# Optimization experiments

Measured on AMD Instinct MI355X. Metric: run time of the kernel, lower is better.

The kernel has to match this reference:

```python
import jax, jax.numpy as jnp
import numpy as np

BN_EPS = 1e-5


def conv1x1(x, W, b):
    # x: [B, Cin, N], W: [Cout, Cin], b: [Cout]
    return jnp.einsum('oc,bcn->bon', W, x) + b[None, :, None]


def bn(x, p):
    # p: [4, C] rows = gamma, beta, running_mean, running_var (inference BN)
    g, be, m, v = p[0], p[1], p[2], p[3]
    inv = jax.lax.rsqrt(v + BN_EPS)
    return (x - m[None, :, None]) * (g * inv)[None, :, None] + be[None, :, None]


def conv_bn_relu(x, W, b, p):
    return jax.nn.relu(bn(conv1x1(x, W, b), p))


def _make_params(key, cout, cin):
    k1, k2 = jax.random.split(key)
    W = jax.random.normal(k1, (cout, cin), jnp.float32) * (1.0 / np.sqrt(cin))
    b = jax.random.normal(k2, (cout,), jnp.float32) * 0.01
    p = jnp.stack([jnp.ones(cout), jnp.zeros(cout), jnp.zeros(cout), jnp.ones(cout)]).astype(jnp.float32)
    return W, b, p


def setup_inputs() -> dict:
    key = jax.random.key(0)
    ks = jax.random.split(key, 16)
    B, N, S, D1, D2 = 2, 16384, 4096, 128, 256
    Cin, C, Cm = D1 + D2 + 13, 128, 128  # 397, out_channel, mlp[0]
    inp = {
        'xyz1': jax.random.normal(ks[0], (B, N, 3), jnp.float32),
        'xyz2': jax.random.normal(ks[1], (B, S, 3), jnp.float32),
        'points1': jax.random.normal(ks[2], (B, D1, N), jnp.float32),
        'points2': jax.random.normal(ks[3], (B, D2, S), jnp.float32),
        'last_pred': jax.random.normal(ks[4], (B, S, 13), jnp.float32),
    }
    inp['fuse_W'], inp['fuse_b'], inp['fuse_bn'] = _make_params(ks[5], C, Cin)
    inp['ext1_W'], inp['ext1_b'], inp['ext1_bn'] = _make_params(ks[6], C, C)
    inp['ext2_W'], inp['ext2_b'], inp['ext2_bn'] = _make_params(ks[7], C, C)
    inp['pred1_W'], inp['pred1_b'], inp['pred1_bn'] = _make_params(ks[8], Cm, C)
    inp['pred2_W'], inp['pred2_b'], inp['pred2_bn'] = _make_params(ks[9], 13, Cm)
    return inp


def _forward(xyz1, xyz2, points1, points2, last_pred,
             fuse_W, fuse_b, fuse_bn, ext1_W, ext1_b, ext1_bn,
             ext2_W, ext2_b, ext2_bn, pred1_W, pred1_b, pred1_bn,
             pred2_W, pred2_b, pred2_bn):
    B, N, _ = xyz1.shape
    p1 = jnp.transpose(points1, (0, 2, 1))  # [B, N, D1]
    p2 = jnp.transpose(points2, (0, 2, 1))  # [B, S, D2]
    # squared distances [B, N, S]
    dists = (jnp.sum(xyz1 ** 2, -1)[:, :, None]
             + jnp.sum(xyz2 ** 2, -1)[:, None, :]
             - 2.0 * jnp.einsum('bnc,bsc->bns', xyz1, xyz2))
    # 3 smallest distances (partial top-k instead of full sort; same math)
    neg_d3, idx = jax.lax.top_k(-dists, 3)  # [B, N, 3]
    d3 = -neg_d3
    recip = 1.0 / (d3 + 1e-8)
    weight = recip / jnp.sum(recip, axis=2, keepdims=True)  # [B, N, 3]
    bidx = jnp.arange(B)[:, None, None]
    interp_pts = jnp.sum(p2[bidx, idx] * weight[..., None], axis=2)        # [B, N, D2]
    interp_pred = jnp.sum(last_pred[bidx, idx] * weight[..., None], axis=2)  # [B, N, 13]
    new_points = jnp.transpose(jnp.concatenate([p1, interp_pts, interp_pred], axis=-1), (0, 2, 1))  # [B, Cin, N]
    # fuse
    x = conv_bn_relu(new_points, fuse_W, fuse_b, fuse_bn)
    # extraction: one ConvBNReLURes1D block (groups=1, res_expansion=1)
    h = conv_bn_relu(x, ext1_W, ext1_b, ext1_bn)
    x = jax.nn.relu(bn(conv1x1(h, ext2_W, ext2_b), ext2_bn) + x)  # [B, C, N]
    new_points_out = x
    # prediction head (dropout is identity in eval mode)
    feat = conv_bn_relu(x, pred1_W, pred1_b, pred1_bn)
    pred = conv_bn_relu(feat, pred2_W, pred2_b, pred2_bn)
    return (new_points_out,
            jnp.transpose(feat, (0, 2, 1)),
            jnp.transpose(pred, (0, 2, 1)))


def reference(xyz1, xyz2, points1, points2, last_pred,
              fuse_W, fuse_b, fuse_bn, ext1_W, ext1_b, ext1_bn,
              ext2_W, ext2_b, ext2_bn, pred1_W, pred1_b, pred1_bn,
              pred2_W, pred2_b, pred2_bn):
    return _forward(xyz1, xyz2, points1, points2, last_pred,
                    fuse_W, fuse_b, fuse_bn, ext1_W, ext1_b, ext1_bn,
                    ext2_W, ext2_b, ext2_bn, pred1_W, pred1_b, pred1_bn,
                    pred2_W, pred2_b, pred2_bn)
```

## Files before the change

### kernel.cpp

```cpp
#include <hip/hip_runtime.h>
#include <stdint.h>

#define B_   2
#define N_   16384
#define S_   4096
#define D2_  256
#define CIN_ 397
#define KP_  416
#define C_   128
#define OC_  13
#define NCHUNK_ 16
#define CHS_ (S_ / NCHUNK_)
#define NCAND_ (NCHUNK_ * 3)
#define XBI_P 296

typedef unsigned short u16;
typedef unsigned int u32;
typedef short s16x8 __attribute__((ext_vector_type(8)));
typedef float f32x4 __attribute__((ext_vector_type(4)));

#define MFMA16(a, b, c) __builtin_amdgcn_mfma_f32_16x16x32_bf16((a), (b), (c), 0, 0, 0)

__device__ __forceinline__ float b2f(u16 h) {
  union { unsigned int u; float f; } v; v.u = ((unsigned int)h) << 16; return v.f;
}
__device__ __forceinline__ u16 f2b(float f) {
  union { float f; unsigned int u; } v; v.f = f;
  unsigned int r = v.u + 0x7fffu + ((v.u >> 16) & 1u);
  return (u16)(r >> 16);
}

#define INS3U32(k0, k1, k2, key)            \
  do {                                      \
    u32 _t1 = max(k0, key);                 \
    u32 _t2 = max(k1, key);                 \
    k0 = min(k0, key);                      \
    k1 = min(k1, _t1);                      \
    k2 = min(k2, _t2);                      \
  } while (0)

__device__ __forceinline__ void transpose_body(
    const float* __restrict__ in, u16* __restrict__ out,
    int C, int S, int opitch, int b, int s0, int c0,
    float* __restrict__ tile, int tr, int tc4) {
  const float* ip = in + (size_t)b * C * S;
  u16* op = out + (size_t)b * S * opitch;
#pragma unroll
  for (int r = 0; r < 64; r += 16) {
    float4 v = *(const float4*)(ip + (size_t)(c0 + tr + r) * S + s0 + tc4);
    tile[(tr + r) * 65 + tc4 + 0] = v.x;
    tile[(tr + r) * 65 + tc4 + 1] = v.y;
    tile[(tr + r) * 65 + tc4 + 2] = v.z;
    tile[(tr + r) * 65 + tc4 + 3] = v.w;
  }
  __syncthreads();
#pragma unroll
  for (int r = 0; r < 64; r += 16) {
    ushort4 v;
    v.x = f2b(tile[(tc4 + 0) * 65 + tr + r]);
    v.y = f2b(tile[(tc4 + 1) * 65 + tr + r]);
    v.z = f2b(tile[(tc4 + 2) * 65 + tr + r]);
    v.w = f2b(tile[(tc4 + 3) * 65 + tr + r]);
    *(ushort4*)(op + (size_t)(s0 + tr + r) * opitch + c0 + tc4) = v;
  }
}

__global__ __launch_bounds__(256) void setup_scan_kernel(
    const float* __restrict__ xyz1, const float* __restrict__ xyz2,
    const float* __restrict__ points1, const float* __restrict__ points2,
    const float* __restrict__ fW, const float* __restrict__ fb,
    const float* __restrict__ fbn,
    const float* __restrict__ e1W, const float* __restrict__ e1b,
    const float* __restrict__ e1bn,
    const float* __restrict__ e2W, const float* __restrict__ e2b,
    const float* __restrict__ e2bn,
    const float* __restrict__ p1W, const float* __restrict__ p1b,
    const float* __restrict__ p1bn,
    const float* __restrict__ p2W, const float* __restrict__ p2b,
    const float* __restrict__ p2bn,
    u16* __restrict__ cand, u16* __restrict__ npT, u16* __restrict__ p2t,
    u16* __restrict__ Wf, u16* __restrict__ W1o,
    u16* __restrict__ W2o, u16* __restrict__ W3o,
    u16* __restrict__ Wp2, float* __restrict__ st) {
  __shared__ __align__(16) float smem[64 * 65];
  int id = blockIdx.x;
  int tid = threadIdx.x;

  if (id < 2048) {
    float4* pts = (float4*)smem;
    int chunk = id & 15;
    int ny = (id >> 4) & 63;
    int b = id >> 10;
    int s0 = chunk * CHS_;
    const float* x2 = xyz2 + ((size_t)b * S_ + s0) * 3;
    {
      float xx = x2[tid * 3], yy = x2[tid * 3 + 1], zz = x2[tid * 3 + 2];
      pts[tid] = make_float4(xx, yy, zz, fmaf(xx, xx, fmaf(yy, yy, zz * zz)));
    }
    __syncthreads();
    int n = ny * 256 + tid;
    const float* x1 = xyz1 + ((size_t)b * N_ + n) * 3;
    float ax = x1[0], ay = x1[1], az = x1[2];
    float n1 = fmaf(ax, ax, fmaf(ay, ay, az * az));
    u32 a0k = 0xFFFFFFFFu, a1k = 0xFFFFFFFFu, a2k = 0xFFFFFFFFu;
    u32 b0k = 0xFFFFFFFFu, b1k = 0xFFFFFFFFu, b2k = 0xFFFFFFFFu;
#pragma unroll 4
    for (int s = 0; s < CHS_; s += 2) {
      float4 p = pts[s];
      float4 q = pts[s + 1];
      float dp = fmaf(ax, p.x, fmaf(ay, p.y, az * p.z));
      float dq = fmaf(ax, q.x, fmaf(ay, q.y, az * q.z));
      float da = fmaxf(fmaf(-2.f, dp, n1 + p.w), 0.f);
      float db = fmaxf(fmaf(-2.f, dq, n1 + q.w), 0.f);
      u32 ka = (__float_as_uint(da) & 0xFFFFFF00u) | (u32)s;
      u32 kb = (__float_as_uint(db) & 0xFFFFFF00u) | (u32)(s + 1);
      INS3U32(a0k, a1k, a2k, ka);
      INS3U32(b0k, b1k, b2k, kb);
    }
    INS3U32(a0k, a1k, a2k, b0k);
    INS3U32(a0k, a1k, a2k, b1k);
    INS3U32(a0k, a1k, a2k, b2k);
    u16* co = cand + ((size_t)(b * N_ + n)) * NCAND_ + chunk * 3;
    co[0] = (u16)((a0k & 0xFFu) + s0);
    co[1] = (u16)((a1k & 0xFFu) + s0);
    co[2] = (u16)((a2k & 0xFFu) + s0);
    return;
  }

  int tr = tid >> 4;
  int tc4 = (tid & 15) * 4;
  if (id < 3072) {
    int id2 = id - 2048;
    int sx = id2 & 255, sy = (id2 >> 8) & 1, b = id2 >> 9;
    transpose_body(points1, npT, 128, N_, 128, b, sx * 64, sy * 64, smem, tr, tc4);
    return;
  }
  if (id < 3584) {
    int id2 = id - 3072;
    int sx = id2 & 63, sy = (id2 >> 6) & 3, b = id2 >> 8;
    transpose_body(points2, p2t, 256, S_, 256, b, sx * 64, sy * 64, smem, tr, tc4);
    return;
  }
  int t = (id - 3584) * 256 + tid;
  int stride = 64 * 256;
  for (int i = t; i < 128 * KP_; i += stride) {
    int m = i / KP_, k = i - m * KP_;
    Wf[i] = (k < CIN_) ? f2b(fW[m * CIN_ + k]) : (u16)0;
  }
  for (int i = t; i < 128 * 128; i += stride) {
    W1o[i] = f2b(e1W[i]);
    W2o[i] = f2b(e2W[i]);
    W3o[i] = f2b(p1W[i]);
  }
  for (int i = t; i < 16 * 128; i += stride) {
    int m = i >> 7;
    Wp2[i] = (m < OC_) ? f2b(p2W[i]) : (u16)0;
  }
  for (int i = t; i < 5 * 128; i += stride) {
    int sg = i >> 7, c = i & 127;
    const float* bn; const float* bc; int Cc = 128;
    switch (sg) {
      case 0: bn = fbn;  bc = fb;  break;
      case 1: bn = e1bn; bc = e1b; break;
      case 2: bn = e2bn; bc = e2b; break;
      case 3: bn = p1bn; bc = p1b; break;
      default: bn = p2bn; bc = p2b; Cc = OC_; break;
    }
    float s = 0.f, tt = 0.f;
    if (c < Cc) {
      float g  = bn[0 * Cc + c], be = bn[1 * Cc + c];
      float mu = bn[2 * Cc + c], vv = bn[3 * Cc + c];
      float inv = 1.0f / sqrtf(vv + 1e-5f);
      s = g * inv;
      tt = (bc[c] - mu) * s + be;
    }
    st[sg * 256 + c] = s;
    st[sg * 256 + 128 + c] = tt;
  }
}

__device__ __forceinline__ void ins3(double d, int i,
                                     double& D0, double& D1, double& D2,
                                     int& I0, int& I1, int& I2) {
  if ((d < D2) || (d == D2 && i < I2)) {
    if ((d < D1) || (d == D1 && i < I1)) {
      D2 = D1; I2 = I1;
      if ((d < D0) || (d == D0 && i < I0)) { D1 = D0; I1 = I0; D0 = d; I0 = i; }
      else                                  { D1 = d; I1 = i; }
    } else { D2 = d; I2 = i; }
  }
}

__device__ __forceinline__ void gemm32(const u16* __restrict__ W, const u16* xb,
                                       int l15, int lq, int wv, f32x4 acc[2][2]) {
#pragma unroll
  for (int mtl = 0; mtl < 2; ++mtl) {
    acc[mtl][0] = (f32x4){0.f, 0.f, 0.f, 0.f};
    acc[mtl][1] = (f32x4){0.f, 0.f, 0.f, 0.f};
  }
#pragma unroll
  for (int ks = 0; ks < 4; ++ks) {
    int ko = ks * 32 + lq * 8;
    s16x8 b0 = *(const s16x8*)(xb + l15 * 136 + ko);
    s16x8 b1 = *(const s16x8*)(xb + (16 + l15) * 136 + ko);
#pragma unroll
    for (int mtl = 0; mtl < 2; ++mtl) {
      s16x8 a = *(const s16x8*)(W + (size_t)((wv * 2 + mtl) * 16 + l15) * 128 + ko);
      acc[mtl][0] = MFMA16(a, b0, acc[mtl][0]);
      acc[mtl][1] = MFMA16(a, b1, acc[mtl][1]);
    }
  }
}

__global__ __launch_bounds__(256, 4) void mega_kernel(
    const float* __restrict__ xyz1, const float* __restrict__ xyz2,
    const u16* __restrict__ cand,
    const u16* __restrict__ npT, const u16* __restrict__ p2t,
    const float* __restrict__ last_pred,
    const u16* __restrict__ Wf,
    const u16* __restrict__ W1, const u16* __restrict__ W2,
    const u16* __restrict__ W3, const u16* __restrict__ Wp2,
    const float* __restrict__ st, float* __restrict__ out) {
  __shared__ __align__(16) u16 xb0[32 * 136];
  __shared__ __align__(16) u16 xb1[32 * 136];
  __shared__ u16 xbi[32 * XBI_P];
  __shared__ float wL[32][3];
  __shared__ int   iL[32][3];
  int b = blockIdx.y;
  int n0 = blockIdx.x * 32;
  int tid = threadIdx.x;
  int wv = tid >> 6, lane = tid & 63;
  int l15 = lane & 15, lq = lane >> 4;
  f32x4 acc[2][2];

  {
#pragma clang fp contract(off)
    double* md = (double*)xb0;
    int*    mi = (int*)xb1;
    int qi = tid >> 3, part = tid & 7;
    int qg = b * N_ + n0 + qi;
    const u16* ci = cand + (size_t)qg * NCAND_ + part * 6;
    const float* x2b = xyz2 + (size_t)b * S_ * 3;
    int ii[6];
#pragma unroll
    for (int j = 0; j < 6; ++j) ii[j] = ci[j];
    float pcx[6], pcy[6], pcz[6];
#pragma unroll
    for (int j = 0; j < 6; ++j) {
      const float* p = x2b + (size_t)ii[j] * 3;
      pcx[j] = p[0]; pcy[j] = p[1]; pcz[j] = p[2];
    }
    const float* x1 = xyz1 + (size_t)qg * 3;
    double ax = x1[0], ay = x1[1], az = x1[2];
    double n1 = (ax * ax + ay * ay) + az * az;
    double D0 = 1e300, D1 = 1e300, D2v = 1e300;
    int I0 = 2147483647, I1 = 2147483647, I2 = 2147483647;
#pragma unroll
    for (int j = 0; j < 6; ++j) {
      double px = pcx[j], py = pcy[j], pz = pcz[j];
      double n2 = (px * px + py * py) + pz * pz;
      double dot = (ax * px + ay * py) + az * pz;
      double d = (n1 + n2) - 2.0 * dot;
      ins3(d, ii[j], D0, D1, D2v, I0, I1, I2);
    }
    md[qi * 24 + part * 3 + 0] = D0; mi[qi * 24 + part * 3 + 0] = I0;
    md[qi * 24 + part * 3 + 1] = D1; mi[qi * 24 + part * 3 + 1] = I1;
    md[qi * 24 + part * 3 + 2] = D2v; mi[qi * 24 + part * 3 + 2] = I2;
  }
  __syncthreads();

  if (tid < 32) {
#pragma clang fp contract(off)
    double* md = (double*)xb0;
    int*    mi = (int*)xb1;
    double D0 = 1e300, D1 = 1e300, D2v = 1e300;
    int I0 = 2147483647, I1 = 2147483647, I2 = 2147483647;
    for (int j = 0; j < 24; ++j) {
      ins3(md[tid * 24 + j], mi[tid * 24 + j], D0, D1, D2v, I0, I1, I2);
    }
    double r0 = 1.0 / (D0 + 1e-8);
    double r1 = 1.0 / (D1 + 1e-8);
    double r2 = 1.0 / (D2v + 1e-8);
    double sum = (r0 + r1) + r2;
    wL[tid][0] = (float)(r0 / sum);
    wL[tid][1] = (float)(r1 / sum);
    wL[tid][2] = (float)(r2 / sum);
    iL[tid][0] = I0; iL[tid][1] = I1; iL[tid][2] = I2;
  }
  __syncthreads();

  {
    const float* lpb = last_pred + (size_t)b * S_ * OC_;
    const u16* p2b = p2t + (size_t)b * S_ * D2_;
    ushort4 g0[8], g1[8], g2[8];
#pragma unroll
    for (int i = 0; i < 8; ++i) {
      int p = wv * 8 + i;
      int i0 = iL[p][0], i1 = iL[p][1], i2 = iL[p][2];
      g0[i] = *(const ushort4*)(p2b + (size_t)i0 * D2_ + lane * 4);
      g1[i] = *(const ushort4*)(p2b + (size_t)i1 * D2_ + lane * 4);
      g2[i] = *(const ushort4*)(p2b + (size_t)i2 * D2_ + lane * 4);
    }
#pragma unroll
    for (int i = 0; i < 8; ++i) {
      int p = wv * 8 + i;
      float w0 = wL[p][0], w1 = wL[p][1], w2 = wL[p][2];
      ushort4 v;
      v.x = f2b((w0 * b2f(g0[i].x) + w1 * b2f(g1[i].x)) + w2 * b2f(g2[i].x));
      v.y = f2b((w0 * b2f(g0[i].y) + w1 * b2f(g1[i].y)) + w2 * b2f(g2[i].y));
      v.z = f2b((w0 * b2f(g0[i].z) + w1 * b2f(g1[i].z)) + w2 * b2f(g2[i].z));
      v.w = f2b((w0 * b2f(g0[i].w) + w1 * b2f(g1[i].w)) + w2 * b2f(g2[i].w));
      *(ushort4*)(&xbi[p * XBI_P + lane * 4]) = v;
      if (lane < 32) {
        u16 pv = 0;
        if (lane < OC_) {
          int i0 = iL[p][0], i1 = iL[p][1], i2 = iL[p][2];
          pv = f2b((w0 * lpb[i0 * OC_ + lane] + w1 * lpb[i1 * OC_ + lane])
                   + w2 * lpb[i2 * OC_ + lane]);
        }
        xbi[p * XBI_P + 256 + lane] = pv;
      }
    }
  }
  __syncthreads();

#pragma unroll
  for (int mtl = 0; mtl < 2; ++mtl) {
    acc[mtl][0] = (f32x4){0.f, 0.f, 0.f, 0.f};
    acc[mtl][1] = (f32x4){0.f, 0.f, 0.f, 0.f};
  }
  {
    const u16* brow0 = npT + ((size_t)(b * N_ + n0 + l15)) * 128;
    const u16* brow1 = brow0 + (size_t)16 * 128;
#pragma unroll 1
    for (int ks = 0; ks < 4; ++ks) {
      int ko = ks * 32 + lq * 8;
      s16x8 bf0 = *(const s16x8*)(brow0 + ko);
      s16x8 bf1 = *(const s16x8*)(brow1 + ko);
#pragma unroll
      for (int mtl = 0; mtl < 2; ++mtl) {
        s16x8 a = *(const s16x8*)(Wf + (size_t)((wv * 2 + mtl) * 16 + l15) * KP_ + ko);
        acc[mtl][0] = MFMA16(a, bf0, acc[mtl][0]);
        acc[mtl][1] = MFMA16(a, bf1, acc[mtl][1]);
      }
    }
#pragma unroll 1
    for (int ks = 0; ks < 9; ++ks) {
      int kk = ks * 32 + lq * 8;
      s16x8 bf0 = *(const s16x8*)(&xbi[l15 * XBI_P + kk]);
      s16x8 bf1 = *(const s16x8*)(&xbi[(16 + l15) * XBI_P + kk]);
#pragma unroll
      for (int mtl = 0; mtl < 2; ++mtl) {
        s16x8 a = *(const s16x8*)(Wf + (size_t)((wv * 2 + mtl) * 16 + l15) * KP_ + 128 + kk);
        acc[mtl][0] = MFMA16(a, bf0, acc[mtl][0]);
        acc[mtl][1] = MFMA16(a, bf1, acc[mtl][1]);
      }
    }
  }
#pragma unroll
  for (int mtl = 0; mtl < 2; ++mtl) {
    int m4 = (wv * 2 + mtl) * 16 + lq * 4;
    f32x4 sc = *(const f32x4*)(st + 0 * 256 + m4);
    f32x4 bi = *(const f32x4*)(st + 0 * 256 + 128 + m4);
#pragma unroll
    for (int nt = 0; nt < 2; ++nt) {
      int n_l = nt * 16 + l15;
      ushort4 v;
      v.x = f2b(fmaxf(acc[mtl][nt][0] * sc[0] + bi[0], 0.f));
      v.y = f2b(fmaxf(acc[mtl][nt][1] * sc[1] + bi[1], 0.f));
      v.z = f2b(fmaxf(acc[mtl][nt][2] * sc[2] + bi[2], 0.f));
      v.w = f2b(fmaxf(acc[mtl][nt][3] * sc[3] + bi[3], 0.f));
      *(ushort4*)(&xb0[n_l * 136 + m4]) = v;
    }
  }
  __syncthreads();

  gemm32(W1, xb0, l15, lq, wv, acc);
#pragma unroll
  for (int mtl = 0; mtl < 2; ++mtl) {
    int m4 = (wv * 2 + mtl) * 16 + lq * 4;
    f32x4 sc = *(const f32x4*)(st + 1 * 256 + m4);
    f32x4 bi = *(const f32x4*)(st + 1 * 256 + 128 + m4);
#pragma unroll
    for (int nt = 0; nt < 2; ++nt) {
      int n_l = nt * 16 + l15;
      ushort4 v;
      v.x = f2b(fmaxf(acc[mtl][nt][0] * sc[0] + bi[0], 0.f));
      v.y = f2b(fmaxf(acc[mtl][nt][1] * sc[1] + bi[1], 0.f));
      v.z = f2b(fmaxf(acc[mtl][nt][2] * sc[2] + bi[2], 0.f));
      v.w = f2b(fmaxf(acc[mtl][nt][3] * sc[3] + bi[3], 0.f));
      *(ushort4*)(&xb1[n_l * 136 + m4]) = v;
    }
  }
  __syncthreads();

  gemm32(W2, xb1, l15, lq, wv, acc);
#pragma unroll
  for (int mtl = 0; mtl < 2; ++mtl) {
    int m4 = (wv * 2 + mtl) * 16 + lq * 4;
    f32x4 sc = *(const f32x4*)(st + 2 * 256 + m4);
    f32x4 bi = *(const f32x4*)(st + 2 * 256 + 128 + m4);
#pragma unroll
    for (int nt = 0; nt < 2; ++nt) {
      int n_l = nt * 16 + l15;
      int n_g = n0 + n_l;
      ushort4 xp = *(const ushort4*)(&xb0[n_l * 136 + m4]);
      float v0 = fmaxf(acc[mtl][nt][0] * sc[0] + bi[0] + b2f(xp.x), 0.f);
      float v1 = fmaxf(acc[mtl][nt][1] * sc[1] + bi[1] + b2f(xp.y), 0.f);
      float v2 = fmaxf(acc[mtl][nt][2] * sc[2] + bi[2] + b2f(xp.z), 0.f);
      float v3 = fmaxf(acc[mtl][nt][3] * sc[3] + bi[3] + b2f(xp.w), 0.f);
      ushort4 v;
      v.x = f2b(v0); v.y = f2b(v1); v.z = f2b(v2); v.w = f2b(v3);
      *(ushort4*)(&xb0[n_l * 136 + m4]) = v;
      out[((size_t)(b * C_ + m4 + 0)) * N_ + n_g] = v0;
      out[((size_t)(b * C_ + m4 + 1)) * N_ + n_g] = v1;
      out[((size_t)(b * C_ + m4 + 2)) * N_ + n_g] = v2;
      out[((size_t)(b * C_ + m4 + 3)) * N_ + n_g] = v3;
    }
  }
  __syncthreads();

  gemm32(W3, xb0, l15, lq, wv, acc);
  {
    float* out1 = out + (size_t)B_ * C_ * N_;
#pragma unroll
    for (int mtl = 0; mtl < 2; ++mtl) {
      int m4 = (wv * 2 + mtl) * 16 + lq * 4;
      f32x4 sc = *(const f32x4*)(st + 3 * 256 + m4);
      f32x4 bi = *(const f32x4*)(st + 3 * 256 + 128 + m4);
#pragma unroll
      for (int nt = 0; nt < 2; ++nt) {
        int n_l = nt * 16 + l15;
        int n_g = n0 + n_l;
        float v0 = fmaxf(acc[mtl][nt][0] * sc[0] + bi[0], 0.f);
        float v1 = fmaxf(acc[mtl][nt][1] * sc[1] + bi[1], 0.f);
        float v2 = fmaxf(acc[mtl][nt][2] * sc[2] + bi[2], 0.f);
        float v3 = fmaxf(acc[mtl][nt][3] * sc[3] + bi[3], 0.f);
        ushort4 v;
        v.x = f2b(v0); v.y = f2b(v1); v.z = f2b(v2); v.w = f2b(v3);
        *(ushort4*)(&xb1[n_l * 136 + m4]) = v;
        float4 o4 = make_float4(v0, v1, v2, v3);
        *(float4*)(out1 + ((size_t)(b * N_ + n_g)) * 128 + m4) = o4;
      }
    }
  }
  __syncthreads();

  if (wv < 2) {
    f32x4 a2 = (f32x4){0.f, 0.f, 0.f, 0.f};
#pragma unroll
    for (int ks = 0; ks < 4; ++ks) {
      int ko = ks * 32 + lq * 8;
      s16x8 b0 = *(const s16x8*)(&xb1[(wv * 16 + l15) * 136 + ko]);
      s16x8 a = *(const s16x8*)(Wp2 + (size_t)l15 * 128 + ko);
      a2 = MFMA16(a, b0, a2);
    }
    float* out2 = out + (size_t)B_ * C_ * N_ + (size_t)B_ * N_ * 128;
    f32x4 sc = *(const f32x4*)(st + 4 * 256 + lq * 4);
    f32x4 bi = *(const f32x4*)(st + 4 * 256 + 128 + lq * 4);
    int n_g = n0 + wv * 16 + l15;
#pragma unroll
    for (int r = 0; r < 4; ++r) {
      int m = lq * 4 + r;
      if (m < OC_) {
        out2[((size_t)(b * N_ + n_g)) * OC_ + m] =
            fmaxf(a2[r] * sc[r] + bi[r], 0.f);
      }
    }
  }
}

extern "C" void kernel_launch(void* const* d_in, const int* in_sizes, int n_in,
                              void* d_out, int out_size, void* d_ws, size_t ws_size,
                              hipStream_t stream) {
  const float* xyz1      = (const float*)d_in[0];
  const float* xyz2      = (const float*)d_in[1];
  const float* points1   = (const float*)d_in[2];
  const float* points2   = (const float*)d_in[3];
  const float* last_pred = (const float*)d_in[4];
  const float* fuse_W    = (const float*)d_in[5];
  const float* fuse_b    = (const float*)d_in[6];
  const float* fuse_bn   = (const float*)d_in[7];
  const float* ext1_W    = (const float*)d_in[8];
  const float* ext1_b    = (const float*)d_in[9];
  const float* ext1_bn   = (const float*)d_in[10];
  const float* ext2_W    = (const float*)d_in[11];
  const float* ext2_b    = (const float*)d_in[12];
  const float* ext2_bn   = (const float*)d_in[13];
  const float* pred1_W   = (const float*)d_in[14];
  const float* pred1_b   = (const float*)d_in[15];
  const float* pred1_bn  = (const float*)d_in[16];
  const float* pred2_W   = (const float*)d_in[17];
  const float* pred2_b   = (const float*)d_in[18];
  const float* pred2_bn  = (const float*)d_in[19];

  char* ws = (char*)d_ws;
  u16*   npT  = (u16*)(ws + 0);
  u16*   p2t  = (u16*)(ws + 8388608);
  u16*   cand = (u16*)(ws + 12582912);
  u16*   Wf   = (u16*)(ws + 15728640);
  u16*   W1   = (u16*)(ws + 15835136);
  u16*   W2   = (u16*)(ws + 15867904);
  u16*   W3   = (u16*)(ws + 15900672);
  u16*   Wp2  = (u16*)(ws + 15933440);
  float* st   = (float*)(ws + 15937536);

  setup_scan_kernel<<<dim3(3648), dim3(256), 0, stream>>>(
      xyz1, xyz2, points1, points2,
      fuse_W, fuse_b, fuse_bn, ext1_W, ext1_b, ext1_bn, ext2_W, ext2_b, ext2_bn,
      pred1_W, pred1_b, pred1_bn, pred2_W, pred2_b, pred2_bn,
      cand, npT, p2t, Wf, W1, W2, W3, Wp2, st);

  mega_kernel<<<dim3(N_ / 32, B_), dim3(256), 0, stream>>>(
      xyz1, xyz2, cand, npT, p2t, last_pred,
      Wf, W1, W2, W3, Wp2, st, (float*)d_out);
}
```

Baseline: 204.8 us.

## Double queries per scan thread and replace LDS top-3 merge with shuffles

The scan kernel now handles two query points per thread against each staged xyz2 chunk, halving scan blocks and reusing each LDS point load twice. In the mega kernel, the per-query top-3 merge across 8 threads is done with xor shuffles instead of shared-memory staging plus a single-lane serial merge, which removes two block barriers. Indices and weights are broadcast with readlane. The points1 tile loads are prefetched at kernel start to overlap the gather phase, at the cost of more registers and possibly lower occupancy.

```diff
diff --git a/kernel.cpp b/kernel.cpp
--- a/kernel.cpp
+++ b/kernel.cpp
@@ -86,11 +86,11 @@
   int id = blockIdx.x;
   int tid = threadIdx.x;
 
-  if (id < 2048) {
+  if (id < 1024) {
     float4* pts = (float4*)smem;
     int chunk = id & 15;
-    int ny = (id >> 4) & 63;
-    int b = id >> 10;
+    int ny = (id >> 4) & 31;
+    int b = id >> 9;
     int s0 = chunk * CHS_;
     const float* x2 = xyz2 + ((size_t)b * S_ + s0) * 3;
     {
@@ -98,50 +98,69 @@
       pts[tid] = make_float4(xx, yy, zz, fmaf(xx, xx, fmaf(yy, yy, zz * zz)));
     }
     __syncthreads();
-    int n = ny * 256 + tid;
-    const float* x1 = xyz1 + ((size_t)b * N_ + n) * 3;
-    float ax = x1[0], ay = x1[1], az = x1[2];
-    float n1 = fmaf(ax, ax, fmaf(ay, ay, az * az));
-    u32 a0k = 0xFFFFFFFFu, a1k = 0xFFFFFFFFu, a2k = 0xFFFFFFFFu;
-    u32 b0k = 0xFFFFFFFFu, b1k = 0xFFFFFFFFu, b2k = 0xFFFFFFFFu;
-#pragma unroll 4
+    int nA = ny * 512 + tid;
+    int nB = nA + 256;
+    const float* x1a = xyz1 + ((size_t)b * N_ + nA) * 3;
+    const float* x1b = xyz1 + ((size_t)b * N_ + nB) * 3;
+    float axA = x1a[0], ayA = x1a[1], azA = x1a[2];
+    float axB = x1b[0], ayB = x1b[1], azB = x1b[2];
+    float n1A = fmaf(axA, axA, fmaf(ayA, ayA, azA * azA));
+    float n1B = fmaf(axB, axB, fmaf(ayB, ayB, azB * azB));
+    u32 a0 = ~0u, a1 = ~0u, a2 = ~0u, b0 = ~0u, b1 = ~0u, b2 = ~0u;
+    u32 c0 = ~0u, c1 = ~0u, c2 = ~0u, d0 = ~0u, d1 = ~0u, d2 = ~0u;
+#pragma unroll 2
     for (int s = 0; s < CHS_; s += 2) {
       float4 p = pts[s];
       float4 q = pts[s + 1];
-      float dp = fmaf(ax, p.x, fmaf(ay, p.y, az * p.z));
-      float dq = fmaf(ax, q.x, fmaf(ay, q.y, az * q.z));
-      float da = fmaxf(fmaf(-2.f, dp, n1 + p.w), 0.f);
-      float db = fmaxf(fmaf(-2.f, dq, n1 + q.w), 0.f);
-      u32 ka = (__float_as_uint(da) & 0xFFFFFF00u) | (u32)s;
-      u32 kb = (__float_as_uint(db) & 0xFFFFFF00u) | (u32)(s + 1);
-      INS3U32(a0k, a1k, a2k, ka);
-      INS3U32(b0k, b1k, b2k, kb);
-    }
-    INS3U32(a0k, a1k, a2k, b0k);
-    INS3U32(a0k, a1k, a2k, b1k);
-    INS3U32(a0k, a1k, a2k, b2k);
-    u16* co = cand + ((size_t)(b * N_ + n)) * NCAND_ + chunk * 3;
-    co[0] = (u16)((a0k & 0xFFu) + s0);
-    co[1] = (u16)((a1k & 0xFFu) + s0);
-    co[2] = (u16)((a2k & 0xFFu) + s0);
+      float dpA = fmaf(axA, p.x, fmaf(ayA, p.y, azA * p.z));
+      float dqA = fmaf(axA, q.x, fmaf(ayA, q.y, azA * q.z));
+      float dpB = fmaf(axB, p.x, fmaf(ayB, p.y, azB * p.z));
+      float dqB = fmaf(axB, q.x, fmaf(ayB, q.y, azB * q.z));
+      float daA = fmaxf(fmaf(-2.f, dpA, n1A + p.w), 0.f);
+      float dbA = fmaxf(fmaf(-2.f, dqA, n1A + q.w), 0.f);
+      float daB = fmaxf(fmaf(-2.f, dpB, n1B + p.w), 0.f);
+      float dbB = fmaxf(fmaf(-2.f, dqB, n1B + q.w), 0.f);
+      u32 kaA = (__float_as_uint(daA) & 0xFFFFFF00u) | (u32)s;
+      u32 kbA = (__float_as_uint(dbA) & 0xFFFFFF00u) | (u32)(s + 1);
+      u32 kaB = (__float_as_uint(daB) & 0xFFFFFF00u) | (u32)s;
+      u32 kbB = (__float_as_uint(dbB) & 0xFFFFFF00u) | (u32)(s + 1);
+      INS3U32(a0, a1, a2, kaA);
+      INS3U32(b0, b1, b2, kbA);
+      INS3U32(c0, c1, c2, kaB);
+      INS3U32(d0, d1, d2, kbB);
+    }
+    INS3U32(a0, a1, a2, b0);
+    INS3U32(a0, a1, a2, b1);
+    INS3U32(a0, a1, a2, b2);
+    INS3U32(c0, c1, c2, d0);
+    INS3U32(c0, c1, c2, d1);
+    INS3U32(c0, c1, c2, d2);
+    u16* coA = cand + ((size_t)(b * N_ + nA)) * NCAND_ + chunk * 3;
+    coA[0] = (u16)((a0 & 0xFFu) + s0);
+    coA[1] = (u16)((a1 & 0xFFu) + s0);
+    coA[2] = (u16)((a2 & 0xFFu) + s0);
+    u16* coB = cand + ((size_t)(b * N_ + nB)) * NCAND_ + chunk * 3;
+    coB[0] = (u16)((c0 & 0xFFu) + s0);
+    coB[1] = (u16)((c1 & 0xFFu) + s0);
+    coB[2] = (u16)((c2 & 0xFFu) + s0);
     return;
   }
 
   int tr = tid >> 4;
   int tc4 = (tid & 15) * 4;
-  if (id < 3072) {
-    int id2 = id - 2048;
+  if (id < 2048) {
+    int id2 = id - 1024;
     int sx = id2 & 255, sy = (id2 >> 8) & 1, b = id2 >> 9;
     transpose_body(points1, npT, 128, N_, 128, b, sx * 64, sy * 64, smem, tr, tc4);
     return;
   }
-  if (id < 3584) {
-    int id2 = id - 3072;
+  if (id < 2560) {
+    int id2 = id - 2048;
     int sx = id2 & 63, sy = (id2 >> 6) & 3, b = id2 >> 8;
     transpose_body(points2, p2t, 256, S_, 256, b, sx * 64, sy * 64, smem, tr, tc4);
     return;
   }
-  int t = (id - 3584) * 256 + tid;
+  int t = (id - 2560) * 256 + tid;
   int stride = 64 * 256;
   for (int i = t; i < 128 * KP_; i += stride) {
     int m = i / KP_, k = i - m * KP_;
@@ -224,8 +243,6 @@
   __shared__ __align__(16) u16 xb0[32 * 136];
   __shared__ __align__(16) u16 xb1[32 * 136];
   __shared__ u16 xbi[32 * XBI_P];
-  __shared__ float wL[32][3];
-  __shared__ int   iL[32][3];
   int b = blockIdx.y;
   int n0 = blockIdx.x * 32;
   int tid = threadIdx.x;
@@ -233,10 +250,22 @@
   int l15 = lane & 15, lq = lane >> 4;
   f32x4 acc[2][2];
 
+  const u16* brow0 = npT + ((size_t)(b * N_ + n0 + l15)) * 128;
+  const u16* brow1 = brow0 + (size_t)16 * 128;
+  s16x8 pf0[4], pf1[4];
+#pragma unroll
+  for (int ks = 0; ks < 4; ++ks) {
+    int ko = ks * 32 + lq * 8;
+    pf0[ks] = *(const s16x8*)(brow0 + ko);
+    pf1[ks] = *(const s16x8*)(brow1 + ko);
+  }
+  __builtin_amdgcn_sched_barrier(0);
+
+  double D0, D1, D2v;
+  int I0, I1, I2;
+  float w0f, w1f, w2f;
   {
 #pragma clang fp contract(off)
-    double* md = (double*)xb0;
-    int*    mi = (int*)xb1;
     int qi = tid >> 3, part = tid & 7;
     int qg = b * N_ + n0 + qi;
     const u16* ci = cand + (size_t)qg * NCAND_ + part * 6;
@@ -250,11 +279,12 @@
       const float* p = x2b + (size_t)ii[j] * 3;
       pcx[j] = p[0]; pcy[j] = p[1]; pcz[j] = p[2];
     }
+    __builtin_amdgcn_sched_barrier(0);
     const float* x1 = xyz1 + (size_t)qg * 3;
     double ax = x1[0], ay = x1[1], az = x1[2];
     double n1 = (ax * ax + ay * ay) + az * az;
-    double D0 = 1e300, D1 = 1e300, D2v = 1e300;
-    int I0 = 2147483647, I1 = 2147483647, I2 = 2147483647;
+    D0 = 1e300; D1 = 1e300; D2v = 1e300;
+    I0 = 2147483647; I1 = 2147483647; I2 = 2147483647;
 #pragma unroll
     for (int j = 0; j < 6; ++j) {
       double px = pcx[j], py = pcy[j], pz = pcz[j];
@@ -263,31 +293,27 @@
       double d = (n1 + n2) - 2.0 * dot;
       ins3(d, ii[j], D0, D1, D2v, I0, I1, I2);
     }
-    md[qi * 24 + part * 3 + 0] = D0; mi[qi * 24 + part * 3 + 0] = I0;
-    md[qi * 24 + part * 3 + 1] = D1; mi[qi * 24 + part * 3 + 1] = I1;
-    md[qi * 24 + part * 3 + 2] = D2v; mi[qi * 24 + part * 3 + 2] = I2;
-  }
-  __syncthreads();
-
-  if (tid < 32) {
-#pragma clang fp contract(off)
-    double* md = (double*)xb0;
-    int*    mi = (int*)xb1;
-    double D0 = 1e300, D1 = 1e300, D2v = 1e300;
-    int I0 = 2147483647, I1 = 2147483647, I2 = 2147483647;
-    for (int j = 0; j < 24; ++j) {
-      ins3(md[tid * 24 + j], mi[tid * 24 + j], D0, D1, D2v, I0, I1, I2);
+#pragma unroll
+    for (int r = 0; r < 3; ++r) {
+      int m = 1 << r;
+      double e0 = __shfl_xor(D0, m);
+      double e1 = __shfl_xor(D1, m);
+      double e2 = __shfl_xor(D2v, m);
+      int j0 = __shfl_xor(I0, m);
+      int j1 = __shfl_xor(I1, m);
+      int j2 = __shfl_xor(I2, m);
+      ins3(e0, j0, D0, D1, D2v, I0, I1, I2);
+      ins3(e1, j1, D0, D1, D2v, I0, I1, I2);
+      ins3(e2, j2, D0, D1, D2v, I0, I1, I2);
     }
     double r0 = 1.0 / (D0 + 1e-8);
     double r1 = 1.0 / (D1 + 1e-8);
     double r2 = 1.0 / (D2v + 1e-8);
     double sum = (r0 + r1) + r2;
-    wL[tid][0] = (float)(r0 / sum);
-    wL[tid][1] = (float)(r1 / sum);
-    wL[tid][2] = (float)(r2 / sum);
-    iL[tid][0] = I0; iL[tid][1] = I1; iL[tid][2] = I2;
-  }
-  __syncthreads();
+    w0f = (float)(r0 / sum);
+    w1f = (float)(r1 / sum);
+    w2f = (float)(r2 / sum);
+  }
 
   {
     const float* lpb = last_pred + (size_t)b * S_ * OC_;
@@ -295,31 +321,35 @@
     ushort4 g0[8], g1[8], g2[8];
 #pragma unroll
     for (int i = 0; i < 8; ++i) {
-      int p = wv * 8 + i;
-      int i0 = iL[p][0], i1 = iL[p][1], i2 = iL[p][2];
+      int i0 = __builtin_amdgcn_readlane(I0, i * 8);
+      int i1 = __builtin_amdgcn_readlane(I1, i * 8);
+      int i2 = __builtin_amdgcn_readlane(I2, i * 8);
       g0[i] = *(const ushort4*)(p2b + (size_t)i0 * D2_ + lane * 4);
       g1[i] = *(const ushort4*)(p2b + (size_t)i1 * D2_ + lane * 4);
       g2[i] = *(const ushort4*)(p2b + (size_t)i2 * D2_ + lane * 4);
     }
+    __builtin_amdgcn_sched_barrier(0);
 #pragma unroll
     for (int i = 0; i < 8; ++i) {
       int p = wv * 8 + i;
-      float w0 = wL[p][0], w1 = wL[p][1], w2 = wL[p][2];
+      float w0 = __uint_as_float(__builtin_amdgcn_readlane(__float_as_uint(w0f), i * 8));
+      float w1 = __uint_as_float(__builtin_amdgcn_readlane(__float_as_uint(w1f), i * 8));
+      float w2 = __uint_as_float(__builtin_amdgcn_readlane(__float_as_uint(w2f), i * 8));
+      int i0 = __builtin_amdgcn_readlane(I0, i * 8);
+      int i1 = __builtin_amdgcn_readlane(I1, i * 8);
+      int i2 = __builtin_amdgcn_readlane(I2, i * 8);
       ushort4 v;
       v.x = f2b((w0 * b2f(g0[i].x) + w1 * b2f(g1[i].x)) + w2 * b2f(g2[i].x));
       v.y = f2b((w0 * b2f(g0[i].y) + w1 * b2f(g1[i].y)) + w2 * b2f(g2[i].y));
       v.z = f2b((w0 * b2f(g0[i].z) + w1 * b2f(g1[i].z)) + w2 * b2f(g2[i].z));
       v.w = f2b((w0 * b2f(g0[i].w) + w1 * b2f(g1[i].w)) + w2 * b2f(g2[i].w));
       *(ushort4*)(&xbi[p * XBI_P + lane * 4]) = v;
-      if (lane < 32) {
-        u16 pv = 0;
-        if (lane < OC_) {
-          int i0 = iL[p][0], i1 = iL[p][1], i2 = iL[p][2];
-          pv = f2b((w0 * lpb[i0 * OC_ + lane] + w1 * lpb[i1 * OC_ + lane])
-                   + w2 * lpb[i2 * OC_ + lane]);
-        }
-        xbi[p * XBI_P + 256 + lane] = pv;
+      u16 pv = 0;
+      if (lane < OC_) {
+        pv = f2b((w0 * lpb[(size_t)i0 * OC_ + lane] + w1 * lpb[(size_t)i1 * OC_ + lane])
+                 + w2 * lpb[(size_t)i2 * OC_ + lane]);
       }
+      if (lane < 32) xbi[p * XBI_P + 256 + lane] = pv;
     }
   }
   __syncthreads();
@@ -330,18 +360,14 @@
     acc[mtl][1] = (f32x4){0.f, 0.f, 0.f, 0.f};
   }
   {
-    const u16* brow0 = npT + ((size_t)(b * N_ + n0 + l15)) * 128;
-    const u16* brow1 = brow0 + (size_t)16 * 128;
-#pragma unroll 1
+#pragma unroll
     for (int ks = 0; ks < 4; ++ks) {
       int ko = ks * 32 + lq * 8;
-      s16x8 bf0 = *(const s16x8*)(brow0 + ko);
-      s16x8 bf1 = *(const s16x8*)(brow1 + ko);
 #pragma unroll
       for (int mtl = 0; mtl < 2; ++mtl) {
         s16x8 a = *(const s16x8*)(Wf + (size_t)((wv * 2 + mtl) * 16 + l15) * KP_ + ko);
-        acc[mtl][0] = MFMA16(a, bf0, acc[mtl][0]);
-        acc[mtl][1] = MFMA16(a, bf1, acc[mtl][1]);
+        acc[mtl][0] = MFMA16(a, pf0[ks], acc[mtl][0]);
+        acc[mtl][1] = MFMA16(a, pf1[ks], acc[mtl][1]);
       }
     }
 #pragma unroll 1
@@ -505,7 +531,7 @@
   u16*   Wp2  = (u16*)(ws + 15933440);
   float* st   = (float*)(ws + 15937536);
 
-  setup_scan_kernel<<<dim3(3648), dim3(256), 0, stream>>>(
+  setup_scan_kernel<<<dim3(2624), dim3(256), 0, stream>>>(
       xyz1, xyz2, points1, points2,
       fuse_W, fuse_b, fuse_bn, ext1_W, ext1_b, ext1_bn, ext2_W, ext2_b, ext2_bn,
       pred1_W, pred1_b, pred1_bn, pred2_W, pred2_b, pred2_bn,
```

New measurement: 207.1 us. No clear change (+1.1%).
